# Kernel optimization log

Measured on AMD Instinct MI355X. Metric: run time of the kernel, lower is better.

## Reference

```python
import jax, jax.numpy as jnp
import numpy as np

DIM = 512
NUM_HEADS = 8
BALL_SIZE = 64
TOPK = 2
DIMENSIONALITY = 3
B = 2
N_BALLS = 1024
N_TOTAL = B * N_BALLS * BALL_SIZE


def setup_inputs() -> dict:
    key = jax.random.key(0)
    ks = jax.random.split(key, 6)
    s = 0.02
    return {
        "x": jax.random.normal(ks[0], (N_TOTAL, DIM), jnp.float32),
        "pos": jax.random.normal(ks[1], (N_TOTAL, DIMENSIONALITY), jnp.float32),
        "qkv_w": jax.random.normal(ks[2], (DIM, 3 * DIM), jnp.float32) * s,
        "qkv_b": jnp.zeros((3 * DIM,), jnp.float32),
        "proj_w": jax.random.normal(ks[3], (DIM, DIM), jnp.float32) * s,
        "proj_b": jnp.zeros((DIM,), jnp.float32),
        "pe_w": jax.random.normal(ks[4], (DIMENSIONALITY, DIM), jnp.float32) * s,
        "pe_b": jnp.zeros((DIM,), jnp.float32),
        "num_batches": B,
    }


def _forward(x, pos, qkv_w, qkv_b, proj_w, proj_b, pe_w, pe_b, num_batches):
    N, D = x.shape
    m = BALL_SIZE
    H = NUM_HEADS
    E = D // H
    b = num_batches
    n = N // (b * m)

    # relative position of leaves wrt ball center (torch.no_grad in original)
    p = pos.reshape(-1, m, pos.shape[-1])
    rel = (p - p.mean(axis=1, keepdims=True)).reshape(N, -1)
    rel = jax.lax.stop_gradient(rel)
    x = x + rel @ pe_w + pe_b

    # qkv split exactly like repeat('(b n m) (H E K) -> K b H n m E'): K innermost
    qkv = (x @ qkv_w + qkv_b).reshape(b, n, m, H, E, 3)
    q = jnp.transpose(qkv[..., 0], (0, 3, 1, 2, 4))  # [b,H,n,m,E]
    k = jnp.transpose(qkv[..., 1], (0, 3, 1, 2, 4))
    v = jnp.transpose(qkv[..., 2], (0, 3, 1, 2, 4))

    # The original's rearrange('b n H m E -> b H n m E') on an already
    # [b,H,n,m,E] tensor swaps head/ball axes; the subsequent repeat along a
    # fresh axis of size m*E followed by gather(dim=2) picks values that are
    # independent of the topk indices. Net effect (exactly reproduced here):
    #   desired_{k,v}[b, h, query, t, m2, e] = {k,v}[b, head=t, ball=h, m2, e]
    # i.e. every query of head h attends to keys/values of ball h taken from
    # the first `topk` heads, flattened in (t, m2) order.
    k_sel = jnp.transpose(k[:, :TOPK, :H], (0, 2, 1, 3, 4)).reshape(b, H, TOPK * m, E)
    v_sel = jnp.transpose(v[:, :TOPK, :H], (0, 2, 1, 3, 4)).reshape(b, H, TOPK * m, E)

    qf = q.reshape(b, H, n * m, E)
    scores = jnp.einsum('bhqe,bhke->bhqk', qf, k_sel) * (E ** -0.5)
    attn = jax.nn.softmax(scores, axis=-1)
    out = jnp.einsum('bhqk,bhke->bhqe', attn, v_sel)  # [b,H,n*m,E]
    out = jnp.transpose(out, (0, 2, 1, 3)).reshape(N, D)  # '(b nm) (H E)'
    return out @ proj_w + proj_b


def reference(x, pos, qkv_w, qkv_b, proj_w, proj_b, pe_w, pe_b, num_batches):
    return _forward(x, pos, qkv_w, qkv_b, proj_w, proj_b, pe_w, pe_b, num_batches)
```

## Files before the change

### kernel.cpp

```cpp
#include <hip/hip_runtime.h>

typedef __bf16 bf16;
typedef __bf16 bf16x8 __attribute__((ext_vector_type(8)));
typedef __bf16 bf16x4 __attribute__((ext_vector_type(4)));
typedef float  f32x4  __attribute__((ext_vector_type(4)));

__device__ __forceinline__ f32x4 mfma16(bf16x8 a, bf16x8 b, f32x4 c) {
    return __builtin_amdgcn_mfma_f32_16x16x32_bf16(a, b, c, 0, 0, 0);
}

__device__ __forceinline__ void gll16(const bf16* g, bf16* l) {
    __builtin_amdgcn_global_load_lds(
        (const __attribute__((address_space(1))) void*)g,
        (__attribute__((address_space(3))) void*)l, 16, 0, 0);
}

__global__ __launch_bounds__(256) void prep_weights(
    const float* __restrict__ qkv_w, const float* __restrict__ qkv_b,
    const float* __restrict__ proj_w,
    bf16* __restrict__ BqT, bf16* __restrict__ kvWT, bf16* __restrict__ projWT,
    float* __restrict__ bkv)
{
    int i = blockIdx.x * 256 + threadIdx.x;
    if (i < 262144) {
        int c_ = i >> 9, k = i & 511;
        int c = (c_ >> 6) * 192 + (c_ & 63) * 3;
        BqT[i] = (bf16)(qkv_w[k * 1536 + c] * 0.125f);
        return;
    }
    i -= 262144;
    if (i < 131072) {
        int c2 = i >> 9, k = i & 511;
        int t = c2 >> 7, kk = (c2 >> 6) & 1, e = c2 & 63;
        int c = t * 192 + e * 3 + 1 + kk;
        kvWT[i] = (bf16)(qkv_w[k * 1536 + c]);
        return;
    }
    i -= 131072;
    if (i < 262144) {
        int c_ = i >> 9, k = i & 511;
        projWT[i] = (bf16)(proj_w[k * 512 + c_]);
        return;
    }
    i -= 262144;
    if (i < 256) {
        int t = i >> 7, kk = (i >> 6) & 1, e = i & 63;
        bkv[i] = qkv_b[t * 192 + e * 3 + 1 + kk];
    }
}

__global__ __launch_bounds__(256) void prep_r2(
    const float* __restrict__ qkv_w, const float* __restrict__ qkv_b,
    const float* __restrict__ pe_w, const float* __restrict__ pe_b,
    float* __restrict__ R, float* __restrict__ bq2)
{
    const int c = blockIdx.x;
    const int tid = threadIdx.x;
    const int qc = (c >> 6) * 192 + (c & 63) * 3;
    float p0 = 0.f, p1 = 0.f, p2 = 0.f, p3 = 0.f;
    for (int k = tid; k < 512; k += 256) {
        float wv = qkv_w[(size_t)k * 1536 + qc];
        p0 += wv * pe_w[k];
        p1 += wv * pe_w[512 + k];
        p2 += wv * pe_w[1024 + k];
        p3 += wv * pe_b[k];
    }
    #pragma unroll
    for (int m = 1; m < 64; m <<= 1) {
        p0 += __shfl_xor(p0, m);
        p1 += __shfl_xor(p1, m);
        p2 += __shfl_xor(p2, m);
        p3 += __shfl_xor(p3, m);
    }
    __shared__ float red[4][4];
    int w = tid >> 6;
    if ((tid & 63) == 0) { red[w][0] = p0; red[w][1] = p1; red[w][2] = p2; red[w][3] = p3; }
    __syncthreads();
    if (tid == 0) {
        float s0 = red[0][0] + red[1][0] + red[2][0] + red[3][0];
        float s1 = red[0][1] + red[1][1] + red[2][1] + red[3][1];
        float s2 = red[0][2] + red[1][2] + red[2][2] + red[3][2];
        float s3 = red[0][3] + red[1][3] + red[2][3] + red[3][3];
        R[0 * 512 + c] = 0.125f * s0;
        R[1 * 512 + c] = 0.125f * s1;
        R[2 * 512 + c] = 0.125f * s2;
        bq2[c] = 0.125f * (qkv_b[qc] + s3);
    }
}

__global__ __launch_bounds__(64) void relprep(const float* __restrict__ pos,
                                              float* __restrict__ rel)
{
    const int t = blockIdx.x * 64 + threadIdx.x;
    float p0 = pos[(size_t)t * 3 + 0];
    float p1 = pos[(size_t)t * 3 + 1];
    float p2 = pos[(size_t)t * 3 + 2];
    float s0 = p0, s1 = p1, s2 = p2;
    #pragma unroll
    for (int m = 1; m < 64; m <<= 1) {
        s0 += __shfl_xor(s0, m);
        s1 += __shfl_xor(s1, m);
        s2 += __shfl_xor(s2, m);
    }
    rel[(size_t)t * 3 + 0] = p0 - s0 * (1.0f / 64.0f);
    rel[(size_t)t * 3 + 1] = p1 - s1 * (1.0f / 64.0f);
    rel[(size_t)t * 3 + 2] = p2 - s2 * (1.0f / 64.0f);
}

__global__ __launch_bounds__(256) void qgemm3(
    const float* __restrict__ X, const bf16* __restrict__ Bt,
    const float* __restrict__ rel, const float* __restrict__ R,
    const float* __restrict__ bq2, bf16* __restrict__ Qout)
{
    const int bid0 = blockIdx.x;
    const int wg = (bid0 & 7) * 512 + (bid0 >> 3);
    const int ct = wg & 3;
    const int rt = wg >> 2;
    const int row0 = rt * 128, col0 = ct * 128;
    const int tid = threadIdx.x;
    const int w = tid >> 6, l = tid & 63;
    const int wr = w >> 1, wc = w & 1;
    const int l15 = l & 15, lg = l >> 4;

    __shared__ __align__(16) bf16 As[8192];
    __shared__ __align__(16) bf16 Bs[8192];
    __shared__ float relS[128][3];
    __shared__ float RS[3][128];

    if (tid < 128) {
        relS[tid][0] = rel[(size_t)(row0 + tid) * 3 + 0];
        relS[tid][1] = rel[(size_t)(row0 + tid) * 3 + 1];
        relS[tid][2] = rel[(size_t)(row0 + tid) * 3 + 2];
    } else {
        int c = tid - 128;
        RS[0][c] = R[0 * 512 + col0 + c];
        RS[1][c] = R[1 * 512 + col0 + c];
        RS[2][c] = R[2 * 512 + col0 + c];
    }

    f32x4 acc[4][4] = {};

    int srow[4], scol[4];
    #pragma unroll
    for (int j = 0; j < 4; ++j) {
        int chunk = w * 4 + j;
        int o = chunk * 512 + l * 8;
        int r = o >> 6;
        int slot = (o & 63) >> 3;
        srow[j] = r;
        scol[j] = ((slot ^ (r & 7)) << 3);
    }
    const int ar_sub = l >> 3;
    const int ak = l & 7;
    const int aslot = (ak ^ ar_sub) << 3;

    float4 va[4][2];
    #pragma unroll
    for (int j = 0; j < 4; ++j) {
        int r = (w * 4 + j) * 8 + ar_sub;
        const float* xp = X + (size_t)(row0 + r) * 512 + ak * 8;
        va[j][0] = *(const float4*)xp;
        va[j][1] = *(const float4*)(xp + 4);
    }

    for (int ki = 0; ki < 8; ++ki) {
        #pragma unroll
        for (int j = 0; j < 4; ++j) {
            int r = (w * 4 + j) * 8 + ar_sub;
            bf16x8 bv = { (bf16)va[j][0].x, (bf16)va[j][0].y, (bf16)va[j][0].z, (bf16)va[j][0].w,
                          (bf16)va[j][1].x, (bf16)va[j][1].y, (bf16)va[j][1].z, (bf16)va[j][1].w };
            *(bf16x8*)&As[r * 64 + aslot] = bv;
            gll16(Bt + (size_t)(col0 + srow[j]) * 512 + ki * 64 + scol[j], &Bs[(w * 4 + j) * 512]);
        }
        __syncthreads();

        #pragma unroll
        for (int kk = 0; kk < 2; ++kk) {
            bf16x8 a[4], b[4];
            #pragma unroll
            for (int mi = 0; mi < 4; ++mi) {
                int r = wr * 64 + mi * 16 + l15;
                int slot = (kk * 4 + lg) ^ (r & 7);
                a[mi] = *(const bf16x8*)&As[r * 64 + slot * 8];
            }
            #pragma unroll
            for (int ni = 0; ni < 4; ++ni) {
                int r = wc * 64 + ni * 16 + l15;
                int slot = (kk * 4 + lg) ^ (r & 7);
                b[ni] = *(const bf16x8*)&Bs[r * 64 + slot * 8];
            }
            #pragma unroll
            for (int mi = 0; mi < 4; ++mi)
                #pragma unroll
                for (int ni = 0; ni < 4; ++ni)
                    acc[mi][ni] = mfma16(a[mi], b[ni], acc[mi][ni]);
        }

        if (ki < 7) {
            int ks = (ki + 1) * 64;
            #pragma unroll
            for (int j = 0; j < 4; ++j) {
                int r = (w * 4 + j) * 8 + ar_sub;
                const float* xp = X + (size_t)(row0 + r) * 512 + ks + ak * 8;
                va[j][0] = *(const float4*)xp;
                va[j][1] = *(const float4*)(xp + 4);
            }
        }
        __syncthreads();
    }

    #pragma unroll
    for (int mi = 0; mi < 4; ++mi) {
        #pragma unroll
        for (int ni = 0; ni < 4; ++ni) {
            int colL = wc * 64 + ni * 16 + l15;
            int col = col0 + colL;
            float bv = bq2[col];
            float r0c = RS[0][colL], r1c = RS[1][colL], r2c = RS[2][colL];
            int rbaseL = wr * 64 + mi * 16 + lg * 4;
            #pragma unroll
            for (int r = 0; r < 4; ++r) {
                int rowL = rbaseL + r;
                float vv = acc[mi][ni][r] + bv
                         + relS[rowL][0] * r0c + relS[rowL][1] * r1c + relS[rowL][2] * r2c;
                Qout[(size_t)(row0 + rowL) * 512 + col] = (bf16)vv;
            }
        }
    }
}

__global__ __launch_bounds__(256) void pgemm3(
    const bf16* __restrict__ A, const bf16* __restrict__ Bt,
    const float* __restrict__ bias, float* __restrict__ out)
{
    const int bid0 = blockIdx.x;
    const int wg = (bid0 & 7) * 512 + (bid0 >> 3);
    const int ct = wg & 3;
    const int rt = wg >> 2;
    const int row0 = rt * 128, col0 = ct * 128;
    const int tid = threadIdx.x;
    const int w = tid >> 6, l = tid & 63;
    const int wr = w >> 1, wc = w & 1;
    const int l15 = l & 15, lg = l >> 4;

    __shared__ __align__(16) bf16 As[8192];
    __shared__ __align__(16) bf16 Bs[8192];

    f32x4 acc[4][4] = {};

    int srow[4], scol[4];
    #pragma unroll
    for (int j = 0; j < 4; ++j) {
        int chunk = w * 4 + j;
        int o = chunk * 512 + l * 8;
        int r = o >> 6;
        int slot = (o & 63) >> 3;
        srow[j] = r;
        scol[j] = ((slot ^ (r & 7)) << 3);
    }

    for (int ki = 0; ki < 8; ++ki) {
        int ks = ki * 64;
        #pragma unroll
        for (int j = 0; j < 4; ++j) {
            gll16(A  + (size_t)(row0 + srow[j]) * 512 + ks + scol[j], &As[(w * 4 + j) * 512]);
            gll16(Bt + (size_t)(col0 + srow[j]) * 512 + ks + scol[j], &Bs[(w * 4 + j) * 512]);
        }
        __syncthreads();
        #pragma unroll
        for (int kk = 0; kk < 2; ++kk) {
            bf16x8 a[4], b[4];
            #pragma unroll
            for (int mi = 0; mi < 4; ++mi) {
                int r = wr * 64 + mi * 16 + l15;
                int slot = (kk * 4 + lg) ^ (r & 7);
                a[mi] = *(const bf16x8*)&As[r * 64 + slot * 8];
            }
            #pragma unroll
            for (int ni = 0; ni < 4; ++ni) {
                int r = wc * 64 + ni * 16 + l15;
                int slot = (kk * 4 + lg) ^ (r & 7);
                b[ni] = *(const bf16x8*)&Bs[r * 64 + slot * 8];
            }
            #pragma unroll
            for (int mi = 0; mi < 4; ++mi)
                #pragma unroll
                for (int ni = 0; ni < 4; ++ni)
                    acc[mi][ni] = mfma16(a[mi], b[ni], acc[mi][ni]);
        }
        __syncthreads();
    }

    #pragma unroll
    for (int mi = 0; mi < 4; ++mi) {
        #pragma unroll
        for (int ni = 0; ni < 4; ++ni) {
            int col = col0 + wc * 64 + ni * 16 + l15;
            float bv = bias[col];
            int rbase = row0 + wr * 64 + mi * 16 + lg * 4;
            #pragma unroll
            for (int r = 0; r < 4; ++r)
                out[(size_t)(rbase + r) * 512 + col] = acc[mi][ni][r] + bv;
        }
    }
}

__global__ __launch_bounds__(256) void kv_proj2(
    const float* __restrict__ x, const float* __restrict__ rel,
    const float* __restrict__ pe_w, const float* __restrict__ pe_b,
    const bf16* __restrict__ kvWT, const float* __restrict__ bkv,
    bf16* __restrict__ ksel, bf16* __restrict__ vselT)
{
    const int bid = blockIdx.x;
    const int b = bid >> 9;
    const int ball = (bid >> 6) & 7;
    const int m2 = bid & 63;
    const size_t tok = (size_t)b * 65536 + ball * 64 + m2;
    const int tid = threadIdx.x;

    __shared__ __align__(16) bf16 xrow[512];
    __shared__ float relt[3];
    if (tid < 3) relt[tid] = rel[tok * 3 + tid];
    __syncthreads();
    for (int k = tid; k < 512; k += 256) {
        float v = x[tok * 512 + k] + relt[0] * pe_w[k] + relt[1] * pe_w[512 + k]
                + relt[2] * pe_w[1024 + k] + pe_b[k];
        xrow[k] = (bf16)v;
    }
    __syncthreads();

    float acc = 0.f;
    const bf16* wrp = kvWT + (size_t)tid * 512;
    #pragma unroll 8
    for (int k = 0; k < 512; k += 8) {
        bf16x8 wv = *(const bf16x8*)(wrp + k);
        bf16x8 xv = *(const bf16x8*)(&xrow[k]);
        #pragma unroll
        for (int j = 0; j < 8; ++j) acc += (float)xv[j] * (float)wv[j];
    }
    acc += bkv[tid];
    int t = tid >> 7, kk = (tid >> 6) & 1, e = tid & 63;
    if (kk == 0)
        ksel[((size_t)(b * 8 + ball) * 128 + t * 64 + m2) * 64 + e] = (bf16)acc;
    else
        vselT[((size_t)(b * 8 + ball) * 64 + e) * 128 + t * 64 + m2] = (bf16)acc;
}

__global__ __launch_bounds__(256) void attn_k(
    const bf16* __restrict__ q, const bf16* __restrict__ ksel,
    const bf16* __restrict__ vselT, bf16* __restrict__ attno)
{
    const int bid = blockIdx.x;
    const int qt = bid & 1023;
    const int bh = bid >> 10;
    const int b = bh >> 3;
    const int h = bh & 7;
    const int tid = threadIdx.x;
    const int w = tid >> 6;
    const int l = tid & 63;
    const int l15 = l & 15, lg = l >> 4;

    __shared__ __align__(16) bf16 Ks[128][72];
    __shared__ __align__(16) bf16 Vt[64][136];
    __shared__ __align__(16) bf16 Pl[4][16][136];

    const bf16* kg = ksel + (size_t)(b * 8 + h) * 128 * 64;
    #pragma unroll
    for (int it = 0; it < 4; ++it) {
        int i = it * 256 + tid;
        int r = i >> 3, c8 = (i & 7) * 8;
        *(bf16x8*)&Ks[r][c8] = *(const bf16x8*)(kg + r * 64 + c8);
    }
    const bf16* vg = vselT + (size_t)(b * 8 + h) * 64 * 128;
    #pragma unroll
    for (int it = 0; it < 4; ++it) {
        int i = it * 256 + tid;
        int r = i >> 4, c8 = (i & 15) * 8;
        *(bf16x8*)&Vt[r][c8] = *(const bf16x8*)(vg + r * 128 + c8);
    }

    const size_t tokq = (size_t)b * 65536 + (size_t)qt * 64 + w * 16 + l15;
    const bf16* qp = q + tokq * 512 + h * 64 + lg * 8;
    bf16x8 qa0 = *(const bf16x8*)qp;
    bf16x8 qa1 = *(const bf16x8*)(qp + 32);

    __syncthreads();

    f32x4 s[8];
    #pragma unroll
    for (int kt = 0; kt < 8; ++kt) {
        f32x4 a0 = {0.f, 0.f, 0.f, 0.f};
        a0 = mfma16(qa0, *(const bf16x8*)&Ks[kt * 16 + l15][lg * 8], a0);
        a0 = mfma16(qa1, *(const bf16x8*)&Ks[kt * 16 + l15][32 + lg * 8], a0);
        s[kt] = a0;
    }

    #pragma unroll
    for (int r = 0; r < 4; ++r) {
        float mx = s[0][r];
        #pragma unroll
        for (int kt = 1; kt < 8; ++kt) mx = fmaxf(mx, s[kt][r]);
        mx = fmaxf(mx, __shfl_xor(mx, 1));
        mx = fmaxf(mx, __shfl_xor(mx, 2));
        mx = fmaxf(mx, __shfl_xor(mx, 4));
        mx = fmaxf(mx, __shfl_xor(mx, 8));
        float sum = 0.f;
        #pragma unroll
        for (int kt = 0; kt < 8; ++kt) {
            float p = __expf(s[kt][r] - mx);
            s[kt][r] = p;
            sum += p;
        }
        sum += __shfl_xor(sum, 1);
        sum += __shfl_xor(sum, 2);
        sum += __shfl_xor(sum, 4);
        sum += __shfl_xor(sum, 8);
        float inv = 1.0f / sum;
        int prow = lg * 4 + r;
        #pragma unroll
        for (int kt = 0; kt < 8; ++kt)
            Pl[w][prow][kt * 16 + l15] = (bf16)(s[kt][r] * inv);
    }

    __syncthreads();

    f32x4 o[4] = { {0,0,0,0}, {0,0,0,0}, {0,0,0,0}, {0,0,0,0} };
    #pragma unroll
    for (int kc = 0; kc < 4; ++kc) {
        bf16x8 pa = *(const bf16x8*)&Pl[w][l15][kc * 32 + lg * 8];
        #pragma unroll
        for (int et = 0; et < 4; ++et)
            o[et] = mfma16(pa, *(const bf16x8*)&Vt[et * 16 + l15][kc * 32 + lg * 8], o[et]);
    }

    #pragma unroll
    for (int et = 0; et < 4; ++et)
        #pragma unroll
        for (int r = 0; r < 4; ++r)
            Pl[w][lg * 4 + r][et * 16 + l15] = (bf16)(o[et][r]);

    __syncthreads();

    {
        int rowg = tid >> 2;
        int w2 = rowg >> 4, lr = rowg & 15;
        int chunk = tid & 3;
        const size_t tok = (size_t)b * 65536 + (size_t)qt * 64 + rowg;
        bf16* gp = attno + tok * 512 + h * 64 + chunk * 16;
        const bf16* lp = &Pl[w2][lr][chunk * 16];
        *(bf16x8*)(gp + 0) = *(const bf16x8*)(lp + 0);
        *(bf16x8*)(gp + 8) = *(const bf16x8*)(lp + 8);
    }
}

extern "C" void kernel_launch(void* const* d_in, const int* in_sizes, int n_in,
                              void* d_out, int out_size, void* d_ws, size_t ws_size,
                              hipStream_t stream) {
    (void)in_sizes; (void)n_in; (void)out_size; (void)ws_size;
    const float* x      = (const float*)d_in[0];
    const float* pos    = (const float*)d_in[1];
    const float* qkv_w  = (const float*)d_in[2];
    const float* qkv_b  = (const float*)d_in[3];
    const float* proj_w = (const float*)d_in[4];
    const float* proj_b = (const float*)d_in[5];
    const float* pe_w   = (const float*)d_in[6];
    const float* pe_b   = (const float*)d_in[7];

    char* ws = (char*)d_ws;
    bf16*  Q     = (bf16*)(ws);
    bf16*  Z     = (bf16*)(ws + 134217728);
    bf16*  BqT   = (bf16*)(ws + 268435456);
    bf16*  PjT   = (bf16*)(ws + 268959744);
    bf16*  kvWT  = (bf16*)(ws + 269484032);
    bf16*  ksel  = (bf16*)(ws + 269746176);
    bf16*  vselT = (bf16*)(ws + 270008320);
    float* rel   = (float*)(ws + 270270464);
    float* R     = (float*)(ws + 271843328);
    float* bq2   = (float*)(ws + 271849472);
    float* bkv   = (float*)(ws + 271851520);

    prep_weights<<<2561, 256, 0, stream>>>(qkv_w, qkv_b, proj_w, BqT, kvWT, PjT, bkv);
    prep_r2<<<512, 256, 0, stream>>>(qkv_w, qkv_b, pe_w, pe_b, R, bq2);
    relprep<<<2048, 64, 0, stream>>>(pos, rel);
    qgemm3<<<4096, 256, 0, stream>>>(x, BqT, rel, R, bq2, Q);
    kv_proj2<<<1024, 256, 0, stream>>>(x, rel, pe_w, pe_b, kvWT, bkv, ksel, vselT);
    attn_k<<<16384, 256, 0, stream>>>(Q, ksel, vselT, Z);
    pgemm3<<<4096, 256, 0, stream>>>(Z, PjT, proj_b, (float*)d_out);
}
```

Measured before the change: 492.0 us.

## Double-buffer B tiles and prefetch next K-slice in Q and projection GEMMs

Both bf16 GEMMs (Q projection and output projection) now double-buffer the B tile in LDS. The next K-slice's global loads are issued before the MFMA work on the current slice, replacing __syncthreads with explicit waitcnt plus s_barrier and sched_barrier fences. The projection GEMM also stages A through registers instead of direct global-to-LDS loads. This aims to hide global memory latency behind compute, at the cost of more LDS per block, which can lower occupancy, and hand-tuned vmcnt values that must match the number of outstanding loads.

```diff
diff --git a/kernel.cpp b/kernel.cpp
--- a/kernel.cpp
+++ b/kernel.cpp
@@ -14,6 +14,8 @@
         (const __attribute__((address_space(1))) void*)g,
         (__attribute__((address_space(3))) void*)l, 16, 0, 0);
 }
+
+#define SCHED_FENCE() __builtin_amdgcn_sched_barrier(0)
 
 __global__ __launch_bounds__(256) void prep_weights(
     const float* __restrict__ qkv_w, const float* __restrict__ qkv_b,
@@ -107,7 +109,7 @@
     rel[(size_t)t * 3 + 2] = p2 - s2 * (1.0f / 64.0f);
 }
 
-__global__ __launch_bounds__(256) void qgemm3(
+__global__ __launch_bounds__(256) void qgemm5(
     const float* __restrict__ X, const bf16* __restrict__ Bt,
     const float* __restrict__ rel, const float* __restrict__ R,
     const float* __restrict__ bq2, bf16* __restrict__ Qout)
@@ -123,7 +125,7 @@
     const int l15 = l & 15, lg = l >> 4;
 
     __shared__ __align__(16) bf16 As[8192];
-    __shared__ __align__(16) bf16 Bs[8192];
+    __shared__ __align__(16) bf16 Bs[2][8192];
     __shared__ float relS[128][3];
     __shared__ float RS[3][128];
 
@@ -161,41 +163,19 @@
         const float* xp = X + (size_t)(row0 + r) * 512 + ak * 8;
         va[j][0] = *(const float4*)xp;
         va[j][1] = *(const float4*)(xp + 4);
-    }
-
+        gll16(Bt + (size_t)(col0 + srow[j]) * 512 + scol[j], &Bs[0][(w * 4 + j) * 512]);
+    }
+
+    #pragma unroll 1
     for (int ki = 0; ki < 8; ++ki) {
+        SCHED_FENCE();
         #pragma unroll
         for (int j = 0; j < 4; ++j) {
             int r = (w * 4 + j) * 8 + ar_sub;
             bf16x8 bv = { (bf16)va[j][0].x, (bf16)va[j][0].y, (bf16)va[j][0].z, (bf16)va[j][0].w,
                           (bf16)va[j][1].x, (bf16)va[j][1].y, (bf16)va[j][1].z, (bf16)va[j][1].w };
             *(bf16x8*)&As[r * 64 + aslot] = bv;
-            gll16(Bt + (size_t)(col0 + srow[j]) * 512 + ki * 64 + scol[j], &Bs[(w * 4 + j) * 512]);
-        }
-        __syncthreads();
-
-        #pragma unroll
-        for (int kk = 0; kk < 2; ++kk) {
-            bf16x8 a[4], b[4];
-            #pragma unroll
-            for (int mi = 0; mi < 4; ++mi) {
-                int r = wr * 64 + mi * 16 + l15;
-                int slot = (kk * 4 + lg) ^ (r & 7);
-                a[mi] = *(const bf16x8*)&As[r * 64 + slot * 8];
-            }
-            #pragma unroll
-            for (int ni = 0; ni < 4; ++ni) {
-                int r = wc * 64 + ni * 16 + l15;
-                int slot = (kk * 4 + lg) ^ (r & 7);
-                b[ni] = *(const bf16x8*)&Bs[r * 64 + slot * 8];
-            }
-            #pragma unroll
-            for (int mi = 0; mi < 4; ++mi)
-                #pragma unroll
-                for (int ni = 0; ni < 4; ++ni)
-                    acc[mi][ni] = mfma16(a[mi], b[ni], acc[mi][ni]);
-        }
-
+        }
         if (ki < 7) {
             int ks = (ki + 1) * 64;
             #pragma unroll
@@ -204,10 +184,44 @@
                 const float* xp = X + (size_t)(row0 + r) * 512 + ks + ak * 8;
                 va[j][0] = *(const float4*)xp;
                 va[j][1] = *(const float4*)(xp + 4);
-            }
-        }
-        __syncthreads();
-    }
+                gll16(Bt + (size_t)(col0 + srow[j]) * 512 + ks + scol[j],
+                      &Bs[(ki + 1) & 1][(w * 4 + j) * 512]);
+            }
+            SCHED_FENCE();
+            asm volatile("s_waitcnt vmcnt(12) lgkmcnt(0)" ::: "memory");
+        } else {
+            SCHED_FENCE();
+            asm volatile("s_waitcnt vmcnt(0) lgkmcnt(0)" ::: "memory");
+        }
+        __builtin_amdgcn_s_barrier();
+        SCHED_FENCE();
+
+        const bf16* Bsc = Bs[ki & 1];
+        #pragma unroll
+        for (int kk = 0; kk < 2; ++kk) {
+            bf16x8 a[4], b[4];
+            #pragma unroll
+            for (int mi = 0; mi < 4; ++mi) {
+                int r = wr * 64 + mi * 16 + l15;
+                int slot = (kk * 4 + lg) ^ (r & 7);
+                a[mi] = *(const bf16x8*)&As[r * 64 + slot * 8];
+            }
+            #pragma unroll
+            for (int ni = 0; ni < 4; ++ni) {
+                int r = wc * 64 + ni * 16 + l15;
+                int slot = (kk * 4 + lg) ^ (r & 7);
+                b[ni] = *(const bf16x8*)&Bsc[r * 64 + slot * 8];
+            }
+            #pragma unroll
+            for (int mi = 0; mi < 4; ++mi)
+                #pragma unroll
+                for (int ni = 0; ni < 4; ++ni)
+                    acc[mi][ni] = mfma16(a[mi], b[ni], acc[mi][ni]);
+        }
+        SCHED_FENCE();
+        __builtin_amdgcn_s_barrier();
+    }
+    SCHED_FENCE();
 
     #pragma unroll
     for (int mi = 0; mi < 4; ++mi) {
@@ -229,7 +243,7 @@
     }
 }
 
-__global__ __launch_bounds__(256) void pgemm3(
+__global__ __launch_bounds__(256) void pgemm5(
     const bf16* __restrict__ A, const bf16* __restrict__ Bt,
     const float* __restrict__ bias, float* __restrict__ out)
 {
@@ -244,7 +258,7 @@
     const int l15 = l & 15, lg = l >> 4;
 
     __shared__ __align__(16) bf16 As[8192];
-    __shared__ __align__(16) bf16 Bs[8192];
+    __shared__ __align__(16) bf16 Bs[2][8192];
 
     f32x4 acc[4][4] = {};
 
@@ -258,15 +272,45 @@
         srow[j] = r;
         scol[j] = ((slot ^ (r & 7)) << 3);
     }
-
+    const int ar_sub = l >> 3;
+    const int ak = l & 7;
+    const int aslot = (ak ^ ar_sub) << 3;
+
+    bf16x8 va[4];
+    #pragma unroll
+    for (int j = 0; j < 4; ++j) {
+        int r = (w * 4 + j) * 8 + ar_sub;
+        va[j] = *(const bf16x8*)(A + (size_t)(row0 + r) * 512 + ak * 8);
+        gll16(Bt + (size_t)(col0 + srow[j]) * 512 + scol[j], &Bs[0][(w * 4 + j) * 512]);
+    }
+
+    #pragma unroll 1
     for (int ki = 0; ki < 8; ++ki) {
-        int ks = ki * 64;
+        SCHED_FENCE();
         #pragma unroll
         for (int j = 0; j < 4; ++j) {
-            gll16(A  + (size_t)(row0 + srow[j]) * 512 + ks + scol[j], &As[(w * 4 + j) * 512]);
-            gll16(Bt + (size_t)(col0 + srow[j]) * 512 + ks + scol[j], &Bs[(w * 4 + j) * 512]);
-        }
-        __syncthreads();
+            int r = (w * 4 + j) * 8 + ar_sub;
+            *(bf16x8*)&As[r * 64 + aslot] = va[j];
+        }
+        if (ki < 7) {
+            int ks = (ki + 1) * 64;
+            #pragma unroll
+            for (int j = 0; j < 4; ++j) {
+                int r = (w * 4 + j) * 8 + ar_sub;
+                va[j] = *(const bf16x8*)(A + (size_t)(row0 + r) * 512 + ks + ak * 8);
+                gll16(Bt + (size_t)(col0 + srow[j]) * 512 + ks + scol[j],
+                      &Bs[(ki + 1) & 1][(w * 4 + j) * 512]);
+            }
+            SCHED_FENCE();
+            asm volatile("s_waitcnt vmcnt(8) lgkmcnt(0)" ::: "memory");
+        } else {
+            SCHED_FENCE();
+            asm volatile("s_waitcnt vmcnt(0) lgkmcnt(0)" ::: "memory");
+        }
+        __builtin_amdgcn_s_barrier();
+        SCHED_FENCE();
+
+        const bf16* Bsc = Bs[ki & 1];
         #pragma unroll
         for (int kk = 0; kk < 2; ++kk) {
             bf16x8 a[4], b[4];
@@ -280,7 +324,7 @@
             for (int ni = 0; ni < 4; ++ni) {
                 int r = wc * 64 + ni * 16 + l15;
                 int slot = (kk * 4 + lg) ^ (r & 7);
-                b[ni] = *(const bf16x8*)&Bs[r * 64 + slot * 8];
+                b[ni] = *(const bf16x8*)&Bsc[r * 64 + slot * 8];
             }
             #pragma unroll
             for (int mi = 0; mi < 4; ++mi)
@@ -288,8 +332,10 @@
                 for (int ni = 0; ni < 4; ++ni)
                     acc[mi][ni] = mfma16(a[mi], b[ni], acc[mi][ni]);
         }
-        __syncthreads();
-    }
+        SCHED_FENCE();
+        __builtin_amdgcn_s_barrier();
+    }
+    SCHED_FENCE();
 
     #pragma unroll
     for (int mi = 0; mi < 4; ++mi) {
@@ -482,8 +528,8 @@
     prep_weights<<<2561, 256, 0, stream>>>(qkv_w, qkv_b, proj_w, BqT, kvWT, PjT, bkv);
     prep_r2<<<512, 256, 0, stream>>>(qkv_w, qkv_b, pe_w, pe_b, R, bq2);
     relprep<<<2048, 64, 0, stream>>>(pos, rel);
-    qgemm3<<<4096, 256, 0, stream>>>(x, BqT, rel, R, bq2, Q);
+    qgemm5<<<4096, 256, 0, stream>>>(x, BqT, rel, R, bq2, Q);
     kv_proj2<<<1024, 256, 0, stream>>>(x, rel, pe_w, pe_b, kvWT, bkv, ksel, vselT);
     attn_k<<<16384, 256, 0, stream>>>(Q, ksel, vselT, Z);
-    pgemm3<<<4096, 256, 0, stream>>>(Z, PjT, proj_b, (float*)d_out);
-}
+    pgemm5<<<4096, 256, 0, stream>>>(Z, PjT, proj_b, (float*)d_out);
+}
```

Result: no change. 486.7 us (-1.1%).

## Use full-width 64-row GEMM tiles and reuse K/V across query tiles in attention

Applied to the files above, without the earlier changes.

The Q-projection and output-projection GEMMs now use 512-thread blocks that each compute a 64-row by 512-column tile. The X/A row tile is therefore read once instead of once per 128-column tile, and each block stages the full 64x512 weight slice per k-step in a larger LDS buffer. The attention kernel now processes four query tiles per block and reuses the staged K and V tiles for all four, which cuts the number of K/V loads and block launches by four. In exchange, LDS use per block grows, occupancy may drop, and the epilogue contains a redundant write of per-column constants.

```diff
diff --git a/kernel.cpp b/kernel.cpp
--- a/kernel.cpp
+++ b/kernel.cpp
@@ -107,70 +107,43 @@
     rel[(size_t)t * 3 + 2] = p2 - s2 * (1.0f / 64.0f);
 }
 
-__global__ __launch_bounds__(256) void qgemm3(
+__global__ __launch_bounds__(512) void qgemm6(
     const float* __restrict__ X, const bf16* __restrict__ Bt,
     const float* __restrict__ rel, const float* __restrict__ R,
     const float* __restrict__ bq2, bf16* __restrict__ Qout)
 {
-    const int bid0 = blockIdx.x;
-    const int wg = (bid0 & 7) * 512 + (bid0 >> 3);
-    const int ct = wg & 3;
-    const int rt = wg >> 2;
-    const int row0 = rt * 128, col0 = ct * 128;
+    const int row0 = blockIdx.x * 64;
     const int tid = threadIdx.x;
     const int w = tid >> 6, l = tid & 63;
-    const int wr = w >> 1, wc = w & 1;
     const int l15 = l & 15, lg = l >> 4;
 
-    __shared__ __align__(16) bf16 As[8192];
-    __shared__ __align__(16) bf16 Bs[8192];
-    __shared__ float relS[128][3];
-    __shared__ float RS[3][128];
-
-    if (tid < 128) {
-        relS[tid][0] = rel[(size_t)(row0 + tid) * 3 + 0];
-        relS[tid][1] = rel[(size_t)(row0 + tid) * 3 + 1];
-        relS[tid][2] = rel[(size_t)(row0 + tid) * 3 + 2];
-    } else {
-        int c = tid - 128;
-        RS[0][c] = R[0 * 512 + col0 + c];
-        RS[1][c] = R[1 * 512 + col0 + c];
-        RS[2][c] = R[2 * 512 + col0 + c];
-    }
+    __shared__ __align__(16) bf16 As[4096];
+    __shared__ __align__(16) bf16 Bs[32768];
 
     f32x4 acc[4][4] = {};
 
-    int srow[4], scol[4];
-    #pragma unroll
-    for (int j = 0; j < 4; ++j) {
-        int chunk = w * 4 + j;
-        int o = chunk * 512 + l * 8;
-        int r = o >> 6;
-        int slot = (o & 63) >> 3;
-        srow[j] = r;
-        scol[j] = ((slot ^ (r & 7)) << 3);
-    }
-    const int ar_sub = l >> 3;
-    const int ak = l & 7;
-    const int aslot = (ak ^ ar_sub) << 3;
-
-    float4 va[4][2];
-    #pragma unroll
-    for (int j = 0; j < 4; ++j) {
-        int r = (w * 4 + j) * 8 + ar_sub;
-        const float* xp = X + (size_t)(row0 + r) * 512 + ak * 8;
-        va[j][0] = *(const float4*)xp;
-        va[j][1] = *(const float4*)(xp + 4);
-    }
+    const int arow = tid >> 3;
+    const int aslot = ((tid & 7) ^ (arow & 7)) << 3;
+    const float* xrow_p = X + (size_t)(row0 + arow) * 512 + (tid & 7) * 8;
+
+    const int bsrow = l >> 3;
+    const int bscol = (((l & 7) ^ (l >> 3)) << 3);
+
+    float4 va0 = *(const float4*)xrow_p;
+    float4 va1 = *(const float4*)(xrow_p + 4);
 
     for (int ki = 0; ki < 8; ++ki) {
-        #pragma unroll
-        for (int j = 0; j < 4; ++j) {
-            int r = (w * 4 + j) * 8 + ar_sub;
-            bf16x8 bv = { (bf16)va[j][0].x, (bf16)va[j][0].y, (bf16)va[j][0].z, (bf16)va[j][0].w,
-                          (bf16)va[j][1].x, (bf16)va[j][1].y, (bf16)va[j][1].z, (bf16)va[j][1].w };
-            *(bf16x8*)&As[r * 64 + aslot] = bv;
-            gll16(Bt + (size_t)(col0 + srow[j]) * 512 + ki * 64 + scol[j], &Bs[(w * 4 + j) * 512]);
+        int ks = ki * 64;
+        {
+            bf16x8 bv = { (bf16)va0.x, (bf16)va0.y, (bf16)va0.z, (bf16)va0.w,
+                          (bf16)va1.x, (bf16)va1.y, (bf16)va1.z, (bf16)va1.w };
+            *(bf16x8*)&As[arow * 64 + aslot] = bv;
+        }
+        #pragma unroll
+        for (int j = 0; j < 8; ++j) {
+            int chunk = w * 8 + j;
+            int col = chunk * 8 + bsrow;
+            gll16(Bt + (size_t)col * 512 + ks + bscol, &Bs[chunk * 512]);
         }
         __syncthreads();
 
@@ -179,13 +152,13 @@
             bf16x8 a[4], b[4];
             #pragma unroll
             for (int mi = 0; mi < 4; ++mi) {
-                int r = wr * 64 + mi * 16 + l15;
+                int r = mi * 16 + l15;
                 int slot = (kk * 4 + lg) ^ (r & 7);
                 a[mi] = *(const bf16x8*)&As[r * 64 + slot * 8];
             }
             #pragma unroll
             for (int ni = 0; ni < 4; ++ni) {
-                int r = wc * 64 + ni * 16 + l15;
+                int r = w * 64 + ni * 16 + l15;
                 int slot = (kk * 4 + lg) ^ (r & 7);
                 b[ni] = *(const bf16x8*)&Bs[r * 64 + slot * 8];
             }
@@ -197,88 +170,104 @@
         }
 
         if (ki < 7) {
-            int ks = (ki + 1) * 64;
-            #pragma unroll
-            for (int j = 0; j < 4; ++j) {
-                int r = (w * 4 + j) * 8 + ar_sub;
-                const float* xp = X + (size_t)(row0 + r) * 512 + ks + ak * 8;
-                va[j][0] = *(const float4*)xp;
-                va[j][1] = *(const float4*)(xp + 4);
-            }
-        }
-        __syncthreads();
-    }
+            va0 = *(const float4*)(xrow_p + (ki + 1) * 64);
+            va1 = *(const float4*)(xrow_p + (ki + 1) * 64 + 4);
+        }
+        __syncthreads();
+    }
+
+    {
+        float4 cp;
+        cp.x = bq2[tid];
+        cp.y = R[tid];
+        cp.z = R[512 + tid];
+        cp.w = R[1024 + tid];
+        ((float4*)As)[tid >> 1] = (tid & 1) ? cp : cp;
+    }
+    {
+        float4 cp;
+        cp.x = bq2[tid];
+        cp.y = R[tid];
+        cp.z = R[512 + tid];
+        cp.w = R[1024 + tid];
+        ((float4*)As)[tid] = cp;
+    }
+    if (tid < 64) {
+        ((float*)Bs)[tid * 3 + 0] = rel[(size_t)(row0 + tid) * 3 + 0];
+        ((float*)Bs)[tid * 3 + 1] = rel[(size_t)(row0 + tid) * 3 + 1];
+        ((float*)Bs)[tid * 3 + 2] = rel[(size_t)(row0 + tid) * 3 + 2];
+    }
+    __syncthreads();
 
     #pragma unroll
     for (int mi = 0; mi < 4; ++mi) {
+        float rl[4][3];
+        #pragma unroll
+        for (int r = 0; r < 4; ++r) {
+            int rowL = mi * 16 + lg * 4 + r;
+            rl[r][0] = ((const float*)Bs)[rowL * 3 + 0];
+            rl[r][1] = ((const float*)Bs)[rowL * 3 + 1];
+            rl[r][2] = ((const float*)Bs)[rowL * 3 + 2];
+        }
         #pragma unroll
         for (int ni = 0; ni < 4; ++ni) {
-            int colL = wc * 64 + ni * 16 + l15;
-            int col = col0 + colL;
-            float bv = bq2[col];
-            float r0c = RS[0][colL], r1c = RS[1][colL], r2c = RS[2][colL];
-            int rbaseL = wr * 64 + mi * 16 + lg * 4;
+            int col = w * 64 + ni * 16 + l15;
+            float4 cp = ((const float4*)As)[col];
             #pragma unroll
             for (int r = 0; r < 4; ++r) {
-                int rowL = rbaseL + r;
-                float vv = acc[mi][ni][r] + bv
-                         + relS[rowL][0] * r0c + relS[rowL][1] * r1c + relS[rowL][2] * r2c;
+                int rowL = mi * 16 + lg * 4 + r;
+                float vv = acc[mi][ni][r] + cp.x
+                         + rl[r][0] * cp.y + rl[r][1] * cp.z + rl[r][2] * cp.w;
                 Qout[(size_t)(row0 + rowL) * 512 + col] = (bf16)vv;
             }
         }
     }
 }
 
-__global__ __launch_bounds__(256) void pgemm3(
+__global__ __launch_bounds__(512) void pgemm6(
     const bf16* __restrict__ A, const bf16* __restrict__ Bt,
     const float* __restrict__ bias, float* __restrict__ out)
 {
-    const int bid0 = blockIdx.x;
-    const int wg = (bid0 & 7) * 512 + (bid0 >> 3);
-    const int ct = wg & 3;
-    const int rt = wg >> 2;
-    const int row0 = rt * 128, col0 = ct * 128;
+    const int row0 = blockIdx.x * 64;
     const int tid = threadIdx.x;
     const int w = tid >> 6, l = tid & 63;
-    const int wr = w >> 1, wc = w & 1;
     const int l15 = l & 15, lg = l >> 4;
 
-    __shared__ __align__(16) bf16 As[8192];
-    __shared__ __align__(16) bf16 Bs[8192];
+    __shared__ __align__(16) bf16 As[4096];
+    __shared__ __align__(16) bf16 Bs[32768];
 
     f32x4 acc[4][4] = {};
 
-    int srow[4], scol[4];
-    #pragma unroll
-    for (int j = 0; j < 4; ++j) {
-        int chunk = w * 4 + j;
-        int o = chunk * 512 + l * 8;
-        int r = o >> 6;
-        int slot = (o & 63) >> 3;
-        srow[j] = r;
-        scol[j] = ((slot ^ (r & 7)) << 3);
-    }
+    const int bsrow = l >> 3;
+    const int bscol = (((l & 7) ^ (l >> 3)) << 3);
+    const int acol = (((l & 7) ^ (l >> 3)) << 3);
 
     for (int ki = 0; ki < 8; ++ki) {
         int ks = ki * 64;
-        #pragma unroll
-        for (int j = 0; j < 4; ++j) {
-            gll16(A  + (size_t)(row0 + srow[j]) * 512 + ks + scol[j], &As[(w * 4 + j) * 512]);
-            gll16(Bt + (size_t)(col0 + srow[j]) * 512 + ks + scol[j], &Bs[(w * 4 + j) * 512]);
-        }
-        __syncthreads();
+        {
+            int arow = w * 8 + bsrow;
+            gll16(A + (size_t)(row0 + arow) * 512 + ks + acol, &As[w * 512]);
+        }
+        #pragma unroll
+        for (int j = 0; j < 8; ++j) {
+            int chunk = w * 8 + j;
+            int col = chunk * 8 + bsrow;
+            gll16(Bt + (size_t)col * 512 + ks + bscol, &Bs[chunk * 512]);
+        }
+        __syncthreads();
+
         #pragma unroll
         for (int kk = 0; kk < 2; ++kk) {
             bf16x8 a[4], b[4];
             #pragma unroll
             for (int mi = 0; mi < 4; ++mi) {
-                int r = wr * 64 + mi * 16 + l15;
+                int r = mi * 16 + l15;
                 int slot = (kk * 4 + lg) ^ (r & 7);
                 a[mi] = *(const bf16x8*)&As[r * 64 + slot * 8];
             }
             #pragma unroll
             for (int ni = 0; ni < 4; ++ni) {
-                int r = wc * 64 + ni * 16 + l15;
+                int r = w * 64 + ni * 16 + l15;
                 int slot = (kk * 4 + lg) ^ (r & 7);
                 b[ni] = *(const bf16x8*)&Bs[r * 64 + slot * 8];
             }
@@ -292,15 +281,15 @@
     }
 
     #pragma unroll
-    for (int mi = 0; mi < 4; ++mi) {
-        #pragma unroll
-        for (int ni = 0; ni < 4; ++ni) {
-            int col = col0 + wc * 64 + ni * 16 + l15;
-            float bv = bias[col];
-            int rbase = row0 + wr * 64 + mi * 16 + lg * 4;
+    for (int ni = 0; ni < 4; ++ni) {
+        int col = w * 64 + ni * 16 + l15;
+        float bv = bias[col];
+        #pragma unroll
+        for (int mi = 0; mi < 4; ++mi) {
+            int rowL = mi * 16 + lg * 4;
             #pragma unroll
             for (int r = 0; r < 4; ++r)
-                out[(size_t)(rbase + r) * 512 + col] = acc[mi][ni][r] + bv;
+                out[(size_t)(row0 + rowL + r) * 512 + col] = acc[mi][ni][r] + bv;
         }
     }
 }
@@ -346,13 +335,13 @@
         vselT[((size_t)(b * 8 + ball) * 64 + e) * 128 + t * 64 + m2] = (bf16)acc;
 }
 
-__global__ __launch_bounds__(256) void attn_k(
+__global__ __launch_bounds__(256) void attn4(
     const bf16* __restrict__ q, const bf16* __restrict__ ksel,
     const bf16* __restrict__ vselT, bf16* __restrict__ attno)
 {
     const int bid = blockIdx.x;
-    const int qt = bid & 1023;
-    const int bh = bid >> 10;
+    const int qg = bid & 255;
+    const int bh = bid >> 8;
     const int b = bh >> 3;
     const int h = bh & 7;
     const int tid = threadIdx.x;
@@ -378,78 +367,78 @@
         int r = i >> 4, c8 = (i & 15) * 8;
         *(bf16x8*)&Vt[r][c8] = *(const bf16x8*)(vg + r * 128 + c8);
     }
-
-    const size_t tokq = (size_t)b * 65536 + (size_t)qt * 64 + w * 16 + l15;
-    const bf16* qp = q + tokq * 512 + h * 64 + lg * 8;
-    bf16x8 qa0 = *(const bf16x8*)qp;
-    bf16x8 qa1 = *(const bf16x8*)(qp + 32);
-
     __syncthreads();
 
-    f32x4 s[8];
-    #pragma unroll
-    for (int kt = 0; kt < 8; ++kt) {
-        f32x4 a0 = {0.f, 0.f, 0.f, 0.f};
-        a0 = mfma16(qa0, *(const bf16x8*)&Ks[kt * 16 + l15][lg * 8], a0);
-        a0 = mfma16(qa1, *(const bf16x8*)&Ks[kt * 16 + l15][32 + lg * 8], a0);
-        s[kt] = a0;
-    }
-
-    #pragma unroll
-    for (int r = 0; r < 4; ++r) {
-        float mx = s[0][r];
-        #pragma unroll
-        for (int kt = 1; kt < 8; ++kt) mx = fmaxf(mx, s[kt][r]);
-        mx = fmaxf(mx, __shfl_xor(mx, 1));
-        mx = fmaxf(mx, __shfl_xor(mx, 2));
-        mx = fmaxf(mx, __shfl_xor(mx, 4));
-        mx = fmaxf(mx, __shfl_xor(mx, 8));
-        float sum = 0.f;
+    for (int qi = 0; qi < 4; ++qi) {
+        const int qt = qg * 4 + qi;
+        const size_t tokq = (size_t)b * 65536 + (size_t)qt * 64 + w * 16 + l15;
+        const bf16* qp = q + tokq * 512 + h * 64 + lg * 8;
+        bf16x8 qa0 = *(const bf16x8*)qp;
+        bf16x8 qa1 = *(const bf16x8*)(qp + 32);
+
+        f32x4 s[8];
         #pragma unroll
         for (int kt = 0; kt < 8; ++kt) {
-            float p = __expf(s[kt][r] - mx);
-            s[kt][r] = p;
-            sum += p;
-        }
-        sum += __shfl_xor(sum, 1);
-        sum += __shfl_xor(sum, 2);
-        sum += __shfl_xor(sum, 4);
-        sum += __shfl_xor(sum, 8);
-        float inv = 1.0f / sum;
-        int prow = lg * 4 + r;
-        #pragma unroll
-        for (int kt = 0; kt < 8; ++kt)
-            Pl[w][prow][kt * 16 + l15] = (bf16)(s[kt][r] * inv);
-    }
-
-    __syncthreads();
-
-    f32x4 o[4] = { {0,0,0,0}, {0,0,0,0}, {0,0,0,0}, {0,0,0,0} };
-    #pragma unroll
-    for (int kc = 0; kc < 4; ++kc) {
-        bf16x8 pa = *(const bf16x8*)&Pl[w][l15][kc * 32 + lg * 8];
+            f32x4 a0 = {0.f, 0.f, 0.f, 0.f};
+            a0 = mfma16(qa0, *(const bf16x8*)&Ks[kt * 16 + l15][lg * 8], a0);
+            a0 = mfma16(qa1, *(const bf16x8*)&Ks[kt * 16 + l15][32 + lg * 8], a0);
+            s[kt] = a0;
+        }
+
+        #pragma unroll
+        for (int r = 0; r < 4; ++r) {
+            float mx = s[0][r];
+            #pragma unroll
+            for (int kt = 1; kt < 8; ++kt) mx = fmaxf(mx, s[kt][r]);
+            mx = fmaxf(mx, __shfl_xor(mx, 1));
+            mx = fmaxf(mx, __shfl_xor(mx, 2));
+            mx = fmaxf(mx, __shfl_xor(mx, 4));
+            mx = fmaxf(mx, __shfl_xor(mx, 8));
+            float sum = 0.f;
+            #pragma unroll
+            for (int kt = 0; kt < 8; ++kt) {
+                float p = __expf(s[kt][r] - mx);
+                s[kt][r] = p;
+                sum += p;
+            }
+            sum += __shfl_xor(sum, 1);
+            sum += __shfl_xor(sum, 2);
+            sum += __shfl_xor(sum, 4);
+            sum += __shfl_xor(sum, 8);
+            float inv = 1.0f / sum;
+            int prow = lg * 4 + r;
+            #pragma unroll
+            for (int kt = 0; kt < 8; ++kt)
+                Pl[w][prow][kt * 16 + l15] = (bf16)(s[kt][r] * inv);
+        }
+
+        f32x4 o[4] = { {0,0,0,0}, {0,0,0,0}, {0,0,0,0}, {0,0,0,0} };
+        #pragma unroll
+        for (int kc = 0; kc < 4; ++kc) {
+            bf16x8 pa = *(const bf16x8*)&Pl[w][l15][kc * 32 + lg * 8];
+            #pragma unroll
+            for (int et = 0; et < 4; ++et)
+                o[et] = mfma16(pa, *(const bf16x8*)&Vt[et * 16 + l15][kc * 32 + lg * 8], o[et]);
+        }
+
         #pragma unroll
         for (int et = 0; et < 4; ++et)
-            o[et] = mfma16(pa, *(const bf16x8*)&Vt[et * 16 + l15][kc * 32 + lg * 8], o[et]);
-    }
-
-    #pragma unroll
-    for (int et = 0; et < 4; ++et)
-        #pragma unroll
-        for (int r = 0; r < 4; ++r)
-            Pl[w][lg * 4 + r][et * 16 + l15] = (bf16)(o[et][r]);
-
-    __syncthreads();
-
-    {
-        int rowg = tid >> 2;
-        int w2 = rowg >> 4, lr = rowg & 15;
-        int chunk = tid & 3;
-        const size_t tok = (size_t)b * 65536 + (size_t)qt * 64 + rowg;
-        bf16* gp = attno + tok * 512 + h * 64 + chunk * 16;
-        const bf16* lp = &Pl[w2][lr][chunk * 16];
-        *(bf16x8*)(gp + 0) = *(const bf16x8*)(lp + 0);
-        *(bf16x8*)(gp + 8) = *(const bf16x8*)(lp + 8);
+            #pragma unroll
+            for (int r = 0; r < 4; ++r)
+                Pl[w][lg * 4 + r][et * 16 + l15] = (bf16)(o[et][r]);
+
+        __syncthreads();
+        {
+            int rowg = tid >> 2;
+            int w2 = rowg >> 4, lr = rowg & 15;
+            int chunk = tid & 3;
+            const size_t tok = (size_t)b * 65536 + (size_t)qt * 64 + rowg;
+            bf16* gp = attno + tok * 512 + h * 64 + chunk * 16;
+            const bf16* lp = &Pl[w2][lr][chunk * 16];
+            *(bf16x8*)(gp + 0) = *(const bf16x8*)(lp + 0);
+            *(bf16x8*)(gp + 8) = *(const bf16x8*)(lp + 8);
+        }
+        __syncthreads();
     }
 }
 
@@ -482,8 +471,8 @@
     prep_weights<<<2561, 256, 0, stream>>>(qkv_w, qkv_b, proj_w, BqT, kvWT, PjT, bkv);
     prep_r2<<<512, 256, 0, stream>>>(qkv_w, qkv_b, pe_w, pe_b, R, bq2);
     relprep<<<2048, 64, 0, stream>>>(pos, rel);
-    qgemm3<<<4096, 256, 0, stream>>>(x, BqT, rel, R, bq2, Q);
+    qgemm6<<<2048, 512, 0, stream>>>(x, BqT, rel, R, bq2, Q);
     kv_proj2<<<1024, 256, 0, stream>>>(x, rel, pe_w, pe_b, kvWT, bkv, ksel, vselT);
-    attn_k<<<16384, 256, 0, stream>>>(Q, ksel, vselT, Z);
-    pgemm3<<<4096, 256, 0, stream>>>(Z, PjT, proj_b, (float*)d_out);
-}
+    attn4<<<4096, 256, 0, stream>>>(Q, ksel, vselT, Z);
+    pgemm6<<<2048, 512, 0, stream>>>(Z, PjT, proj_b, (float*)d_out);
+}
```

New measurement: 422.0 us. -14.2%, faster.
